# Optimization experiments

Measured on AMD Instinct MI355X. Metric: run time of the kernel, lower is better.

## Reference

```python
import jax, jax.numpy as jnp
import numpy as np

B, N2, N3, D = 16, 1024, 2048, 128


def setup_inputs() -> dict:
    key = jax.random.key(0)
    k1, k2 = jax.random.split(key)
    desc2d = jax.random.normal(k1, (B * N2, D), dtype=jnp.float32)
    desc3d = jax.random.normal(k2, (B * N3, D), dtype=jnp.float32)
    # uniform, sorted batch ids (equal-size segments -> jit-friendly ragged layout)
    idx2d = jnp.repeat(jnp.arange(B, dtype=jnp.int64), N2)
    idx3d = jnp.repeat(jnp.arange(B, dtype=jnp.int64), N3)
    return {"desc2d": desc2d, "idx2d": idx2d, "desc3d": desc3d, "idx3d": idx3d}


def reference(desc2d, idx2d, desc3d, idx3d):
    # number of batches from sorted batch ids (static, computed on host)
    nb = int(np.asarray(idx2d)[-1]) + 1
    n2 = desc2d.shape[0] // nb
    n3 = desc3d.shape[0] // nb
    d2 = desc2d.reshape(nb, n2, -1)  # [B, n2, D]
    d3 = desc3d.reshape(nb, n3, -1)  # [B, n3, D]
    d2 = d2 / jnp.linalg.norm(d2, axis=-1, keepdims=True)
    d3 = d3 / jnp.linalg.norm(d3, axis=-1, keepdims=True)
    sim = jnp.einsum('bid,bjd->bij', d3, d2)  # cosine similarity [B, n3, n2]
    # zero-pad one extra row and column per batch (dustbin), as in the original
    return jnp.pad(sim, ((0, 0), (0, 1), (0, 1)))
```

## Files before the change

### kernel.cpp

```cpp
#include <hip/hip_runtime.h>
#include <hip/hip_bf16.h>

#define NB   16
#define N2   1024
#define N3   2048
#define DD   128
#define OROWS (N3 + 1)
#define OCOLS (N2 + 1)

typedef __attribute__((ext_vector_type(8))) __bf16 bf16x8;
typedef __attribute__((ext_vector_type(4))) float  f32x4;

static __device__ __forceinline__ unsigned pack_bf16x2(float a, float b) {
    unsigned ua = __float_as_uint(a);
    ua = (ua + 0x7FFF + ((ua >> 16) & 1)) >> 16;
    unsigned ub = __float_as_uint(b);
    ub = (ub + 0x7FFF + ((ub >> 16) & 1)) & 0xFFFF0000u;
    return ua | ub;
}

__global__ void normalize_d2(const float* __restrict__ d2,
                             unsigned short* __restrict__ ws) {
    const int row = blockIdx.x * 8 + (threadIdx.x >> 5);
    const int l   = threadIdx.x & 31;
    const float4 v = *reinterpret_cast<const float4*>(d2 + (size_t)row * DD + l * 4);
    float ss = v.x * v.x + v.y * v.y + v.z * v.z + v.w * v.w;
    #pragma unroll
    for (int off = 16; off; off >>= 1) ss += __shfl_xor(ss, off);
    const float s = rsqrtf(ss);
    uint2 w;
    w.x = pack_bf16x2(v.x * s, v.y * s);
    w.y = pack_bf16x2(v.z * s, v.w * s);
    *reinterpret_cast<uint2*>(ws + (size_t)row * DD + l * 4) = w;
}

__global__ __launch_bounds__(256, 2)
void gemm_kernel(const float* __restrict__ d3,
                 const unsigned short* __restrict__ d2n,
                 float* __restrict__ out) {
    __shared__ __align__(16) char smem[65536];

    const int hw  = blockIdx.x;
    const int blk = (hw & 7) * 64 + (hw >> 3);
    const int b   = blk >> 5;
    const int ti  = blk & 31;
    const int t   = threadIdx.x;

    const float* gA = d3 + (size_t)(b * N3 + ti * 64) * DD;
    const char*  gB = (const char*)d2n + ((size_t)(b * N2) << 8);

    char* const aLds = smem + 49152;

    auto stage = [&](int c) {
        const char* src = gB + (size_t)c * 16384;
        char* dst = smem + 16384 * ((c + 2) % 3);
        #pragma unroll
        for (int it = 0; it < 4; ++it) {
            int o    = it * 4096 + t * 16;
            int row  = o >> 8;
            int scol = (o & 255) ^ ((row & 7) << 4);
            __builtin_amdgcn_global_load_lds(
                (const __attribute__((address_space(1))) void*)(src + row * 256 + scol),
                (__attribute__((address_space(3))) void*)(dst + o), 16, 0, 0);
        }
    };

    const int arow  = t >> 2;
    const int apart = t & 3;
    float4 av[8];
    #pragma unroll
    for (int i = 0; i < 8; ++i)
        av[i] = *reinterpret_cast<const float4*>(gA + (size_t)arow * DD + apart * 32 + i * 4);
    stage(0);

    {
        float ss = 0.f;
        #pragma unroll
        for (int i = 0; i < 8; ++i)
            ss += av[i].x * av[i].x + av[i].y * av[i].y + av[i].z * av[i].z + av[i].w * av[i].w;
        ss += __shfl_xor(ss, 1);
        ss += __shfl_xor(ss, 2);
        const float s = rsqrtf(ss);
        const int aswz = (arow & 7) << 4;
        #pragma unroll
        for (int j = 0; j < 4; ++j) {
            uint4 w;
            w.x = pack_bf16x2(av[2 * j].x * s,     av[2 * j].y * s);
            w.y = pack_bf16x2(av[2 * j].z * s,     av[2 * j].w * s);
            w.z = pack_bf16x2(av[2 * j + 1].x * s, av[2 * j + 1].y * s);
            w.w = pack_bf16x2(av[2 * j + 1].z * s, av[2 * j + 1].w * s);
            int colb = apart * 64 + j * 16;
            *reinterpret_cast<uint4*>(aLds + arow * 256 + (colb ^ aswz)) = w;
        }
    }
    asm volatile("s_waitcnt vmcnt(0) lgkmcnt(0)" ::: "memory");
    __builtin_amdgcn_s_barrier();
    __builtin_amdgcn_sched_barrier(0);

    const int wid = t >> 6;
    const int l   = t & 63;
    const int wm  = wid * 16;
    const int lr  = l & 15;
    const int kq  = l >> 4;
    const int sw  = (lr & 7) << 4;

    bf16x8 af[4];
    #pragma unroll
    for (int ks = 0; ks < 4; ++ks) {
        const int kb = ks * 64 + kq * 16;
        af[ks] = *reinterpret_cast<const bf16x8*>(aLds + (wm + lr) * 256 + (kb ^ sw));
    }

    float* obase = out + (size_t)b * OROWS * OCOLS + (size_t)(ti * 64) * OCOLS;

    for (int nj = 0; nj < 16; ++nj) {
        const char* bbuf = smem + 16384 * ((nj + 2) % 3);

        f32x4 acc[4] = {};
        #pragma unroll
        for (int ks = 0; ks < 4; ++ks) {
            const int kb = ks * 64 + kq * 16;
            #pragma unroll
            for (int ni = 0; ni < 4; ++ni) {
                bf16x8 bfr = *reinterpret_cast<const bf16x8*>(
                    bbuf + (ni * 16 + lr) * 256 + (kb ^ sw));
                acc[ni] = __builtin_amdgcn_mfma_f32_16x16x32_bf16(
                    af[ks], bfr, acc[ni], 0, 0, 0);
            }
        }

        if (nj == 0) { stage(1); stage(2); }
        else if (nj + 2 < 16) stage(nj + 2);

        #pragma unroll
        for (int i = 0; i < 4; ++i) {
            int r = wm + kq * 4 + i;
            #pragma unroll
            for (int ni = 0; ni < 4; ++ni) {
                int c = nj * 64 + ni * 16 + lr;
                obase[(size_t)r * OCOLS + c] = acc[ni][i];
            }
        }

        if (nj < 14) {
            asm volatile("s_waitcnt vmcnt(20)" ::: "memory");
            __builtin_amdgcn_s_barrier();
            __builtin_amdgcn_sched_barrier(0);
        } else if (nj == 14) {
            asm volatile("s_waitcnt vmcnt(16)" ::: "memory");
            __builtin_amdgcn_s_barrier();
            __builtin_amdgcn_sched_barrier(0);
        }
    }

    if (t < 64)
        obase[(size_t)t * OCOLS + N2] = 0.0f;
    if (ti == 31) {
        float* last = out + (size_t)b * OROWS * OCOLS + (size_t)N3 * OCOLS;
        for (int c = t; c < OCOLS; c += 256) last[c] = 0.0f;
    }
}

extern "C" void kernel_launch(void* const* d_in, const int* in_sizes, int n_in,
                              void* d_out, int out_size, void* d_ws, size_t ws_size,
                              hipStream_t stream) {
    (void)in_sizes; (void)n_in; (void)out_size; (void)ws_size;
    const float* desc2d = (const float*)d_in[0];
    const float* desc3d = (const float*)d_in[2];

    unsigned short* d2n = (unsigned short*)d_ws;
    float* out = (float*)d_out;

    normalize_d2<<<(NB * N2) / 8, 256, 0, stream>>>(desc2d, d2n);
    gemm_kernel<<<NB * (N3 / 64), 256, 0, stream>>>(desc3d, d2n, out);
}
```

Baseline: 40.39 us.

## Stage output tiles through LDS to emit aligned 16-byte global stores

Each wave now writes its 16x64 accumulator tile into a per-wave LDS scratch area, using the freed A-operand LDS, with a rotation that accounts for the row misalignment caused by the odd row stride of 1025. It then reads the tile back and issues 16-byte vector stores aligned to the row's offset, with scalar edge stores at the ends. This replaces scattered 4-byte stores and is meant to improve write coalescing on this output-bound kernel. In exchange it adds LDS traffic, divergent edge-handling code, and full __syncthreads barriers that replace the fine-grained vmcnt waits, which may weaken the overlap with the B prefetch.

```diff
diff --git a/kernel.cpp b/kernel.cpp
--- a/kernel.cpp
+++ b/kernel.cpp
@@ -93,9 +93,7 @@
             *reinterpret_cast<uint4*>(aLds + arow * 256 + (colb ^ aswz)) = w;
         }
     }
-    asm volatile("s_waitcnt vmcnt(0) lgkmcnt(0)" ::: "memory");
-    __builtin_amdgcn_s_barrier();
-    __builtin_amdgcn_sched_barrier(0);
+    __syncthreads();
 
     const int wid = t >> 6;
     const int l   = t & 63;
@@ -111,7 +109,11 @@
         af[ks] = *reinterpret_cast<const bf16x8*>(aLds + (wm + lr) * 256 + (kb ^ sw));
     }
 
+    char* const tscratch = aLds + wid * 4096;
     float* obase = out + (size_t)b * OROWS * OCOLS + (size_t)(ti * 64) * OCOLS;
+
+    const int li  = lr;
+    const int a_r = (4 - ((b + kq) & 3)) & 3;
 
     for (int nj = 0; nj < 16; ++nj) {
         const char* bbuf = smem + 16384 * ((nj + 2) % 3);
@@ -133,24 +135,43 @@
         else if (nj + 2 < 16) stage(nj + 2);
 
         #pragma unroll
-        for (int i = 0; i < 4; ++i) {
-            int r = wm + kq * 4 + i;
+        for (int ni = 0; ni < 4; ++ni) {
             #pragma unroll
-            for (int ni = 0; ni < 4; ++ni) {
-                int c = nj * 64 + ni * 16 + lr;
-                obase[(size_t)r * OCOLS + c] = acc[ni][i];
+            for (int i = 0; i < 4; ++i) {
+                int R   = kq * 4 + i;
+                int a_w = (4 - ((b + i) & 3)) & 3;
+                int cd  = ((ni * 16 + lr) + 4 * R - a_w) & 63;
+                *reinterpret_cast<float*>(tscratch + R * 256 + cd * 4) = acc[ni][i];
             }
         }
 
-        if (nj < 14) {
-            asm volatile("s_waitcnt vmcnt(20)" ::: "memory");
-            __builtin_amdgcn_s_barrier();
-            __builtin_amdgcn_sched_barrier(0);
-        } else if (nj == 14) {
-            asm volatile("s_waitcnt vmcnt(16)" ::: "memory");
-            __builtin_amdgcn_s_barrier();
-            __builtin_amdgcn_sched_barrier(0);
+        #pragma unroll
+        for (int j = 0; j < 4; ++j) {
+            int R = j * 4 + kq;
+            float* rowp = obase + (size_t)(wm + R) * OCOLS + nj * 64;
+            if (li < 15) {
+                f32x4 v = *reinterpret_cast<const f32x4*>(
+                    tscratch + R * 256 + ((4 * li + 4 * R) & 63) * 4);
+                *reinterpret_cast<f32x4*>(rowp + a_r + 4 * li) = v;
+            } else if (a_r == 0) {
+                f32x4 v = *reinterpret_cast<const f32x4*>(
+                    tscratch + R * 256 + ((60 + 4 * R) & 63) * 4);
+                *reinterpret_cast<f32x4*>(rowp + 60) = v;
+            } else {
+                #pragma unroll
+                for (int k = 0; k < 3; ++k)
+                    if (k < a_r)
+                        rowp[k] = *reinterpret_cast<const float*>(
+                            tscratch + R * 256 + ((k - a_r + 64 + 4 * R) & 63) * 4);
+                #pragma unroll
+                for (int k = 0; k < 4; ++k)
+                    if (k < 4 - a_r)
+                        rowp[60 + a_r + k] = *reinterpret_cast<const float*>(
+                            tscratch + R * 256 + ((60 + k + 4 * R) & 63) * 4);
+            }
         }
+
+        __syncthreads();
     }
 
     if (t < 64)
```

Measured after the change: 52.56 us. +30.1%, slower.

## Fuse d2 normalization into GEMM kernel via cooperative launch and grid sync

Applied to the files above, without the earlier changes.

Folds the separate desc2d normalize-to-bf16 kernel into the GEMM kernel as a prologue: each of the 512 blocks normalizes 32 rows of d2, then all blocks meet at a cooperative grid-wide sync before the GEMM reads the normalized workspace. This removes one kernel launch and the gap between the two kernels. In exchange it needs a cooperative launch, which requires every block to be co-resident, and it adds the cost of a grid barrier. It also loses the overlap of the d3 loads with the normalization phase.

```diff
diff --git a/kernel.cpp b/kernel.cpp
--- a/kernel.cpp
+++ b/kernel.cpp
@@ -1,5 +1,8 @@
 #include <hip/hip_runtime.h>
 #include <hip/hip_bf16.h>
+#include <hip/hip_cooperative_groups.h>
+
+namespace cg = cooperative_groups;
 
 #define NB   16
 #define N2   1024
@@ -19,32 +22,43 @@
     return ua | ub;
 }
 
-__global__ void normalize_d2(const float* __restrict__ d2,
-                             unsigned short* __restrict__ ws) {
-    const int row = blockIdx.x * 8 + (threadIdx.x >> 5);
-    const int l   = threadIdx.x & 31;
-    const float4 v = *reinterpret_cast<const float4*>(d2 + (size_t)row * DD + l * 4);
-    float ss = v.x * v.x + v.y * v.y + v.z * v.z + v.w * v.w;
-    #pragma unroll
-    for (int off = 16; off; off >>= 1) ss += __shfl_xor(ss, off);
-    const float s = rsqrtf(ss);
-    uint2 w;
-    w.x = pack_bf16x2(v.x * s, v.y * s);
-    w.y = pack_bf16x2(v.z * s, v.w * s);
-    *reinterpret_cast<uint2*>(ws + (size_t)row * DD + l * 4) = w;
-}
-
 __global__ __launch_bounds__(256, 2)
-void gemm_kernel(const float* __restrict__ d3,
-                 const unsigned short* __restrict__ d2n,
-                 float* __restrict__ out) {
+void fused_kernel(const float* __restrict__ d2,
+                  const float* __restrict__ d3,
+                  unsigned short* __restrict__ d2n,
+                  float* __restrict__ out) {
     __shared__ __align__(16) char smem[65536];
 
-    const int hw  = blockIdx.x;
+    const int hw = blockIdx.x;
+    const int t  = threadIdx.x;
+
+    {
+        const int x   = hw & 7;
+        const int idx = hw >> 3;
+        const int nb_ = 2 * x + (idx >> 5);
+        const int r0  = (idx & 31) * 32;
+        const float* src = d2 + ((size_t)nb_ * N2 + r0) * DD;
+        unsigned short* dst = d2n + ((size_t)nb_ * N2 + r0) * DD;
+        #pragma unroll
+        for (int p = 0; p < 4; ++p) {
+            const int row = p * 8 + (t >> 5);
+            const int l   = t & 31;
+            const float4 v = *reinterpret_cast<const float4*>(src + (size_t)row * DD + l * 4);
+            float ss = v.x * v.x + v.y * v.y + v.z * v.z + v.w * v.w;
+            #pragma unroll
+            for (int off = 16; off; off >>= 1) ss += __shfl_xor(ss, off);
+            const float s = rsqrtf(ss);
+            uint2 w;
+            w.x = pack_bf16x2(v.x * s, v.y * s);
+            w.y = pack_bf16x2(v.z * s, v.w * s);
+            *reinterpret_cast<uint2*>(dst + (size_t)row * DD + l * 4) = w;
+        }
+    }
+    cg::this_grid().sync();
+
     const int blk = (hw & 7) * 64 + (hw >> 3);
     const int b   = blk >> 5;
     const int ti  = blk & 31;
-    const int t   = threadIdx.x;
 
     const float* gA = d3 + (size_t)(b * N3 + ti * 64) * DD;
     const char*  gB = (const char*)d2n + ((size_t)(b * N2) << 8);
@@ -171,6 +185,7 @@
     unsigned short* d2n = (unsigned short*)d_ws;
     float* out = (float*)d_out;
 
-    normalize_d2<<<(NB * N2) / 8, 256, 0, stream>>>(desc2d, d2n);
-    gemm_kernel<<<NB * (N3 / 64), 256, 0, stream>>>(desc3d, d2n, out);
+    void* args[] = { (void*)&desc2d, (void*)&desc3d, (void*)&d2n, (void*)&out };
+    hipLaunchCooperativeKernel((void*)fused_kernel, dim3(NB * (N3 / 64)),
+                               dim3(256), args, 0, stream);
 }
```

New measurement: 87.10 us. 2.16x slower.
